# Optimization experiments

Hardware: AMD Instinct MI355X
Metric: run time of the kernel (lower is better)

The kernel has to match this reference:

```python
import jax, jax.numpy as jnp
import numpy as np

MAX_LORAS = 16
D_IN = 4096
D_OUT = 64
B = 32
S = 2048


def setup_inputs() -> dict:
    key = jax.random.key(0)
    k1, k2, k3 = jax.random.split(key, 3)
    x = jax.random.normal(k1, (B, S, D_IN), dtype=jnp.float32)
    adapter_ids = jax.random.randint(k2, (B,), 0, MAX_LORAS)
    # weight table: (max_loras, input_size, output_size) since memory_transpose=True
    weight = jax.random.normal(k3, (MAX_LORAS, D_IN, D_OUT), dtype=jnp.float32) * 0.02
    return {"x": x, "adapter_ids": adapter_ids, "weight": weight}


def reference(x, adapter_ids, weight):
    # get_weight: gather per-sample weight [B, D_IN, D_OUT]
    weights = weight[adapter_ids]
    # memory_transpose=True path: einsum('bij,bjk->bik')
    return jnp.einsum('bij,bjk->bik', x, weights)
```

## Files before the change

kernel.cpp:

```cpp
#include <hip/hip_runtime.h>

#define DIN 4096
#define DOUT 64
#define SEQ 2048
#define BK 64
#define WT_STRIDE 72

typedef __bf16 bf16x8 __attribute__((ext_vector_type(8)));
typedef float f32x4 __attribute__((ext_vector_type(4)));

__global__ __launch_bounds__(256, 2)
void lora_gemm_kernel(const float* __restrict__ x,
                      const int* __restrict__ adapter_ids,
                      const float* __restrict__ weight,
                      float* __restrict__ out)
{
    __shared__ __align__(16) __bf16 wt[64 * WT_STRIDE];

    const int bid  = blockIdx.x;
    const int row0 = bid * 64;
    const int b    = row0 / SEQ;
    const int aid  = adapter_ids[b];
    const float* wbase = weight + (size_t)aid * DIN * DOUT;

    const int tid  = threadIdx.x;
    const int wave = tid >> 6;
    const int lane = tid & 63;
    const int m16  = lane & 15;
    const int quad = lane >> 4;

    const float* xrow = x + (size_t)(row0 + wave * 16 + m16) * DIN + quad * 8;

    f32x4 acc[4];
#pragma unroll
    for (int t = 0; t < 4; ++t) acc[t] = (f32x4)0.0f;

    const int s_kk = tid >> 4;
    const int s_n4 = tid & 15;

    for (int k0 = 0; k0 < DIN; k0 += BK) {
#pragma unroll
        for (int p = 0; p < 4; ++p) {
            const int kk = p * 16 + s_kk;
            const f32x4 w4 = *(const f32x4*)(wbase + (size_t)(k0 + kk) * DOUT + s_n4 * 4);
#pragma unroll
            for (int i = 0; i < 4; ++i)
                wt[(s_n4 * 4 + i) * WT_STRIDE + kk] = (__bf16)w4[i];
        }
        __syncthreads();

#pragma unroll
        for (int ks = 0; ks < BK; ks += 32) {
            const f32x4 xa = *(const f32x4*)(xrow + k0 + ks);
            const f32x4 xb = *(const f32x4*)(xrow + k0 + ks + 4);
            bf16x8 a;
            a[0] = (__bf16)xa[0]; a[1] = (__bf16)xa[1];
            a[2] = (__bf16)xa[2]; a[3] = (__bf16)xa[3];
            a[4] = (__bf16)xb[0]; a[5] = (__bf16)xb[1];
            a[6] = (__bf16)xb[2]; a[7] = (__bf16)xb[3];
#pragma unroll
            for (int t = 0; t < 4; ++t) {
                const bf16x8 bf = *(const bf16x8*)(&wt[(t * 16 + m16) * WT_STRIDE + ks + quad * 8]);
                acc[t] = __builtin_amdgcn_mfma_f32_16x16x32_bf16(a, bf, acc[t], 0, 0, 0);
            }
        }
        __syncthreads();
    }

    float* obase = out + (size_t)(row0 + wave * 16 + quad * 4) * DOUT + m16;
#pragma unroll
    for (int i = 0; i < 4; ++i)
#pragma unroll
        for (int t = 0; t < 4; ++t)
            obase[(size_t)i * DOUT + t * 16] = acc[t][i];
}

extern "C" void kernel_launch(void* const* d_in, const int* in_sizes, int n_in,
                              void* d_out, int out_size, void* d_ws, size_t ws_size,
                              hipStream_t stream) {
    const float* x   = (const float*)d_in[0];
    const int*   ids = (const int*)d_in[1];
    const float* w   = (const float*)d_in[2];
    float* out = (float*)d_out;

    const int total_rows = 32 * SEQ;
    dim3 grid(total_rows / 64);
    dim3 block(256);
    lora_gemm_kernel<<<grid, block, 0, stream>>>(x, ids, w, out);
}
```

Before: 1.383 ms.

## Prepack LoRA weights into MFMA-fragment bf16 layout and drop LDS staging

Adds a prep kernel that converts the fp32 weight table to bf16 in the exact per-lane MFMA B-fragment order in workspace. The main GEMM then loads each fragment directly from global memory (L2-resident) with no shared memory and no barriers, and uses higher occupancy. This removes the per-tile LDS transpose and sync overhead, at the cost of an extra kernel launch and a workspace pass over the weights. It falls back to the old LDS kernel when no workspace is available.

```diff
diff --git a/kernel.cpp b/kernel.cpp
--- a/kernel.cpp
+++ b/kernel.cpp
@@ -3,17 +3,90 @@
 #define DIN 4096
 #define DOUT 64
 #define SEQ 2048
+#define MAXL 16
+#define NSLAB (DIN / 32)
 #define BK 64
 #define WT_STRIDE 72
 
 typedef __bf16 bf16x8 __attribute__((ext_vector_type(8)));
 typedef float f32x4 __attribute__((ext_vector_type(4)));
 
+__global__ __launch_bounds__(256)
+void lora_wprep(const float* __restrict__ weight, __bf16* __restrict__ wpre)
+{
+    const int bid  = blockIdx.x;
+    const int tid  = threadIdx.x;
+    const int t    = tid >> 6;
+    const int lane = tid & 63;
+    const int aid  = bid >> 7;
+    const int s    = bid & (NSLAB - 1);
+
+    const float* src = weight
+        + ((size_t)aid * DIN + s * 32 + (lane >> 4) * 8) * DOUT
+        + t * 16 + (lane & 15);
+
+    bf16x8 v;
+#pragma unroll
+    for (int j = 0; j < 8; ++j)
+        v[j] = (__bf16)src[(size_t)j * DOUT];
+
+    *((bf16x8*)wpre + ((size_t)bid * 4 + t) * 64 + lane) = v;
+}
+
+__global__ __launch_bounds__(256, 4)
+void lora_gemm_fast(const float* __restrict__ x,
+                    const int* __restrict__ adapter_ids,
+                    const __bf16* __restrict__ wpre,
+                    float* __restrict__ out)
+{
+    const int bid  = blockIdx.x;
+    const int row0 = bid * 64;
+    const int b    = row0 / SEQ;
+    const int aid  = adapter_ids[b];
+
+    const int tid  = threadIdx.x;
+    const int wave = tid >> 6;
+    const int lane = tid & 63;
+    const int m16  = lane & 15;
+    const int quad = lane >> 4;
+
+    const float*  xrow = x + (size_t)(row0 + wave * 16 + m16) * DIN + quad * 8;
+    const bf16x8* wp   = (const bf16x8*)wpre + (size_t)aid * NSLAB * 4 * 64 + lane;
+
+    f32x4 acc[4];
+#pragma unroll
+    for (int t = 0; t < 4; ++t) acc[t] = (f32x4)0.0f;
+
+#pragma unroll 2
+    for (int s = 0; s < NSLAB; ++s) {
+        const f32x4 xa = *(const f32x4*)(xrow + s * 32);
+        const f32x4 xb = *(const f32x4*)(xrow + s * 32 + 4);
+        bf16x8 a;
+        a[0] = (__bf16)xa[0]; a[1] = (__bf16)xa[1];
+        a[2] = (__bf16)xa[2]; a[3] = (__bf16)xa[3];
+        a[4] = (__bf16)xb[0]; a[5] = (__bf16)xb[1];
+        a[6] = (__bf16)xb[2]; a[7] = (__bf16)xb[3];
+
+#pragma unroll
+        for (int t = 0; t < 4; ++t) {
+            const bf16x8 bf = wp[(s * 4 + t) * 64];
+            acc[t] = __builtin_amdgcn_mfma_f32_16x16x32_bf16(a, bf, acc[t], 0, 0, 0);
+        }
+    }
+
+    float* obase = out + (size_t)(row0 + wave * 16 + quad * 4) * DOUT + m16;
+#pragma unroll
+    for (int i = 0; i < 4; ++i)
+#pragma unroll
+        for (int t = 0; t < 4; ++t)
+            obase[(size_t)i * DOUT + t * 16] = acc[t][i];
+}
+
 __global__ __launch_bounds__(256, 2)
-void lora_gemm_kernel(const float* __restrict__ x,
-                      const int* __restrict__ adapter_ids,
-                      const float* __restrict__ weight,
-                      float* __restrict__ out)
+void lora_gemm_lds(const float* __restrict__ x,
+                   const int* __restrict__ adapter_ids,
+                   const float* __restrict__ weight,
+                   float* __restrict__ out)
 {
     __shared__ __align__(16) __bf16 wt[64 * WT_STRIDE];
 
@@ -81,10 +154,16 @@
     const float* x   = (const float*)d_in[0];
     const int*   ids = (const int*)d_in[1];
     const float* w   = (const float*)d_in[2];
-    float* out = (float*)d_out;
+    float* out       = (float*)d_out;
 
     const int total_rows = 32 * SEQ;
-    dim3 grid(total_rows / 64);
-    dim3 block(256);
-    lora_gemm_kernel<<<grid, block, 0, stream>>>(x, ids, w, out);
+    const size_t wpre_bytes = (size_t)MAXL * DIN * DOUT * sizeof(__bf16);
+
+    if (d_ws != nullptr && ws_size >= wpre_bytes) {
+        __bf16* wpre = (__bf16*)d_ws;
+        lora_wprep<<<dim3(MAXL * NSLAB), dim3(256), 0, stream>>>(w, wpre);
+        lora_gemm_fast<<<dim3(total_rows / 64), dim3(256), 0, stream>>>(x, ids, wpre, out);
+    } else {
+        lora_gemm_lds<<<dim3(total_rows / 64), dim3(256), 0, stream>>>(x, ids, w, out);
+    }
 }
```

Result: slower. 1.413 ms (+2.2%).
